# Performance work log

Hardware: AMD Instinct MI355X
Metric: run time of the kernel (lower is better)

The kernel has to match this reference:

```python
import jax, jax.numpy as jnp
import numpy as np

E, TOPK = 32, 2            # hardcoded in LossMOEDecoder
D, HID, BOT, OUT = 768, 2048, 256, 768
B, S = 2, 128


def setup_inputs() -> dict:
    key = jax.random.key(0)
    ks = jax.random.split(key, 7)
    p = lambda k, shape: jax.random.normal(k, shape, dtype=jnp.float32) * 0.02
    return {
        "x": jax.random.normal(ks[0], (B, S, D), dtype=jnp.float32),
        "gate_w": p(ks[1], (E, D)),                 # MoEGate.weight
        "W1": p(ks[2], (E, D, HID)),  "b1": jnp.zeros((E, HID), jnp.float32),
        "W2": p(ks[3], (E, HID, HID)), "b2": jnp.zeros((E, HID), jnp.float32),
        "W3": p(ks[4], (E, HID, BOT)), "b3": jnp.zeros((E, BOT), jnp.float32),
        "Wl": p(ks[5], (E, BOT, OUT)), "bl": jnp.zeros((E, OUT), jnp.float32),
    }


def reference(x, gate_w, W1, b1, W2, b2, W3, b3, Wl, bl):
    Bz, Sl, d = x.shape
    xt = x.reshape(-1, d)                                    # [N, d] tokens
    # --- gate: softmax then top-k (values permutation-invariant vs torch sorted=False)
    scores = jax.nn.softmax(xt @ gate_w.T, axis=-1)          # [N, E]
    topk_w, topk_idx = jax.lax.top_k(scores, TOPK)           # [N, k]
    topk_w = topk_w / (topk_w.sum(-1, keepdims=True) + 1e-20)  # norm_topk_prob
    # --- experts: batched over the (small, fixed) expert axis; exact GELU as nn.GELU
    gelu = lambda v: jax.nn.gelu(v, approximate=False)
    h = gelu(jnp.einsum('nd,edh->enh', xt, W1) + b1[:, None, :])   # [E, N, HID]
    h = gelu(jnp.einsum('enh,ehg->eng', h, W2) + b2[:, None, :])   # [E, N, HID]
    z = jnp.einsum('eng,egb->enb', h, W3) + b3[:, None, :]         # [E, N, BOT]
    out_all = jnp.einsum('enb,ebo->eno', z, Wl) + bl[:, None, :]   # [E, N, OUT]
    # --- combine: gather each token's top-k expert outputs, weighted sum
    sel = jnp.take_along_axis(out_all.transpose(1, 0, 2),          # [N, E, OUT]
                              topk_idx[:, :, None], axis=1)        # [N, k, OUT]
    y = (sel * topk_w[:, :, None]).sum(axis=1)                     # [N, OUT]
    return y.reshape(Bz, Sl, OUT)
```

## Files before the change

### kernel.cpp

```cpp
#include <hip/hip_runtime.h>
#include <math.h>

#define NEXP 32
#define NTOK 256
#define DIMD 768
#define DHID 2048
#define DBOT 256
#define DOUT 768
#define NSLOT 512

__global__ __launch_bounds__(64) void gate_kernel(
    const float* __restrict__ x, const float* __restrict__ gw,
    int* __restrict__ topk_idx, float* __restrict__ topk_w) {
  const int n = blockIdx.x;
  const int l = threadIdx.x;
  const float* xr = x + n * DIMD;
  float xs[12];
#pragma unroll
  for (int j = 0; j < 12; j++) xs[j] = xr[l + 64 * j];
  float logit[NEXP];
#pragma unroll
  for (int e = 0; e < NEXP; e++) {
    const float* g = gw + e * DIMD;
    float p = 0.f;
#pragma unroll
    for (int j = 0; j < 12; j++) p = fmaf(xs[j], g[l + 64 * j], p);
#pragma unroll
    for (int m = 1; m < 64; m <<= 1) p += __shfl_xor(p, m);
    logit[e] = p;
  }
  int i0 = 0; float m0 = logit[0];
#pragma unroll
  for (int e = 1; e < NEXP; e++) { if (logit[e] > m0) { m0 = logit[e]; i0 = e; } }
  int i1 = -1; float m1 = -3.4e38f;
#pragma unroll
  for (int e = 0; e < NEXP; e++) { if (e != i0 && logit[e] > m1) { m1 = logit[e]; i1 = e; } }
  const float e1 = expf(m1 - m0);
  const float w0 = 1.f / (1.f + e1);
  const float w1 = e1 * w0;
  if (l == 0) {
    topk_idx[2 * n] = i0; topk_idx[2 * n + 1] = i1;
    topk_w[2 * n] = w0;  topk_w[2 * n + 1] = w1;
  }
}

__global__ __launch_bounds__(256) void build_lists(
    const int* __restrict__ topk_idx,
    int* __restrict__ counts, int* __restrict__ offsets,
    int* __restrict__ tok_list, int* __restrict__ tok2slot,
    int* __restrict__ slot_expert) {
  __shared__ int cnt[NEXP], base[NEXP], fill[NEXP];
  const int t = threadIdx.x;
  if (t < NEXP) { cnt[t] = 0; fill[t] = 0; }
  __syncthreads();
  const int e0 = topk_idx[2 * t], e1 = topk_idx[2 * t + 1];
  atomicAdd(&cnt[e0], 1);
  atomicAdd(&cnt[e1], 1);
  __syncthreads();
  if (t == 0) { int s = 0; for (int i = 0; i < NEXP; i++) { base[i] = s; s += cnt[i]; } }
  __syncthreads();
  const int p0 = atomicAdd(&fill[e0], 1);
  tok_list[base[e0] + p0] = t; tok2slot[2 * t] = base[e0] + p0;
  slot_expert[base[e0] + p0] = e0;
  const int p1 = atomicAdd(&fill[e1], 1);
  tok_list[base[e1] + p1] = t; tok2slot[2 * t + 1] = base[e1] + p1;
  slot_expert[base[e1] + p1] = e1;
  if (t < NEXP) { counts[t] = cnt[t]; offsets[t] = base[t]; }
}

__device__ __forceinline__ float gelu_f(float v) {
  return 0.5f * v * (1.f + erff(v * 0.70710678118654752f));
}

__global__ __launch_bounds__(64) void zsum_kernel(
    const float* __restrict__ zpart, const float* __restrict__ b3,
    const int* __restrict__ slot_expert, float* __restrict__ zsum) {
  const int slot = blockIdx.x;
  const int c = threadIdx.x * 4;
  const int e = slot_expert[slot];
  float4 q = *(const float4*)(b3 + (size_t)e * DBOT + c);
#pragma unroll
  for (int k = 0; k < 8; k++) {
    const float4 p = *(const float4*)(zpart + ((size_t)k * NSLOT + slot) * DBOT + c);
    q.x += p.x; q.y += p.y; q.z += p.z; q.w += p.w;
  }
  *(float4*)(zsum + (size_t)slot * DBOT + c) = q;
}

#define FMA4(A, XS, WV) \
  A.x = fmaf(XS, WV.x, A.x); A.y = fmaf(XS, WV.y, A.y); \
  A.z = fmaf(XS, WV.z, A.z); A.w = fmaf(XS, WV.w, A.w)

template <int MODE>
__global__ __launch_bounds__(512, 2) void ff_kernel(
    const float* __restrict__ Ain, const float* __restrict__ W,
    const float* __restrict__ Bias, float* __restrict__ Out,
    const int* __restrict__ offsets, const int* __restrict__ counts,
    const int* __restrict__ tok_list) {
  constexpr int NCT   = (MODE <= 1) ? 2048 : (MODE == 2) ? 256 : 768;
  constexpr int KFULL = (MODE == 0) ? 768 : (MODE == 3) ? 256 : 2048;
  constexpr int INS   = (MODE == 0) ? DIMD : (MODE == 3) ? DBOT : DHID;
  constexpr int NSEC  = (MODE == 0) ? 12 : (MODE == 1) ? 32 : 4;
  __shared__ float Wlds[2 * 64 * 256];
  __shared__ float act_t[2 * 64 * 32];
  const int tid  = threadIdx.x;
  const int lane = tid & 63;
  const int wave = tid >> 6;
  const int tg   = wave;
  const int e    = blockIdx.y;
  const int kb   = (MODE == 2) ? blockIdx.x : 0;
  const int ct   = (MODE == 2) ? 0 : blockIdx.x;
  const int kbase = kb * 256;
  const int cnt = counts[e];
  const int off = offsets[e];
  const int col = ct * 256 + lane * 4;
  const float* Wsrc = W + ((size_t)e * KFULL) * NCT + (size_t)ct * 256;
  const int tok = tid & 31;
  const int kk  = tid >> 5;

  for (int tc0 = 0; tc0 < cnt; tc0 += 32) {
    const int tcn = min(32, cnt - tc0);
    const int slot = off + tc0 + tok;
    const float* Arow = nullptr;
    if (tok < tcn) {
      const int row = (MODE == 0) ? tok_list[slot] : slot;
      Arow = Ain + (size_t)row * INS + kbase;
    }

    float4 acc[4];
#pragma unroll
    for (int t = 0; t < 4; t++) acc[t] = {0.f, 0.f, 0.f, 0.f};
    float4 av = {0.f, 0.f, 0.f, 0.f};

    auto a_issue = [&](int s) {
      if (Arow) av = *(const float4*)(Arow + s * 64 + kk * 4);
      else      av = {0.f, 0.f, 0.f, 0.f};
    };
    auto w_issue = [&](int b, int s) {
      float* wl = Wlds + b * 16384;
      const float* src = Wsrc + (size_t)(kbase + s * 64) * NCT;
#pragma unroll
      for (int c = 0; c < 8; c++) {
        const int r = c * 8 + wave;
        __builtin_amdgcn_global_load_lds(
            (const __attribute__((address_space(1))) void*)(src + (size_t)r * NCT + lane * 4),
            (__attribute__((address_space(3))) void*)(wl + r * 256),
            16, 0, 0);
      }
    };
    auto a_write = [&](int b) {
      float* at = act_t + b * 2048;
      at[(kk * 4 + 0) * 32 + tok] = av.x;
      at[(kk * 4 + 1) * 32 + tok] = av.y;
      at[(kk * 4 + 2) * 32 + tok] = av.z;
      at[(kk * 4 + 3) * 32 + tok] = av.w;
    };

    a_issue(0);
    w_issue(0, 0);
    a_write(0);
    __syncthreads();

    for (int s = 0; s < NSEC; s++) {
      const int b = s & 1;
      if (s + 1 < NSEC) {
        a_issue(s + 1);
        w_issue(b ^ 1, s + 1);
      }
      {
        const float* wl = Wlds + b * 16384 + lane * 4;
        const float* at = act_t + b * 2048 + tg * 4;
#pragma unroll 8
        for (int r = 0; r < 64; r++) {
          const float4 wv = *(const float4*)(wl + r * 256);
          const float4 xv = *(const float4*)(at + r * 32);
          FMA4(acc[0], xv.x, wv);
          FMA4(acc[1], xv.y, wv);
          FMA4(acc[2], xv.z, wv);
          FMA4(acc[3], xv.w, wv);
        }
      }
      if (s + 1 < NSEC) a_write(b ^ 1);
      __syncthreads();
    }

    float4 bv = {0.f, 0.f, 0.f, 0.f};
    if (MODE <= 1) bv = *(const float4*)(Bias + (size_t)e * NCT + col);
#pragma unroll
    for (int tt = 0; tt < 4; tt++) {
      if (tg * 4 + tt < tcn) {
        const int os = off + tc0 + tg * 4 + tt;
        float4 o = acc[tt];
        if (MODE <= 1) {
          o.x = gelu_f(o.x + bv.x); o.y = gelu_f(o.y + bv.y);
          o.z = gelu_f(o.z + bv.z); o.w = gelu_f(o.w + bv.w);
          *(float4*)(Out + (size_t)os * NCT + col) = o;
        } else if (MODE == 2) {
          *(float4*)(Out + ((size_t)kb * NSLOT + os) * DBOT + col) = o;
        } else {
          *(float4*)(Out + (size_t)os * DOUT + col) = o;
        }
      }
    }
    __syncthreads();
  }
}

__global__ __launch_bounds__(192) void combine_kernel(
    const float* __restrict__ OutS, const float* __restrict__ bl,
    const int* __restrict__ topk_idx, const float* __restrict__ topk_w,
    const int* __restrict__ tok2slot, float* __restrict__ y) {
  const int n = blockIdx.x;
  const int c = threadIdx.x * 4;
  const int s0 = tok2slot[2 * n], s1 = tok2slot[2 * n + 1];
  const int e0 = topk_idx[2 * n], e1 = topk_idx[2 * n + 1];
  const float w0 = topk_w[2 * n], w1 = topk_w[2 * n + 1];
  const float4 a  = *(const float4*)(OutS + (size_t)s0 * DOUT + c);
  const float4 b  = *(const float4*)(OutS + (size_t)s1 * DOUT + c);
  const float4 ba = *(const float4*)(bl + (size_t)e0 * DOUT + c);
  const float4 bb = *(const float4*)(bl + (size_t)e1 * DOUT + c);
  float4 o;
  o.x = w0 * (a.x + ba.x) + w1 * (b.x + bb.x);
  o.y = w0 * (a.y + ba.y) + w1 * (b.y + bb.y);
  o.z = w0 * (a.z + ba.z) + w1 * (b.z + bb.z);
  o.w = w0 * (a.w + ba.w) + w1 * (b.w + bb.w);
  *(float4*)(y + (size_t)n * DOUT + c) = o;
}

extern "C" void kernel_launch(void* const* d_in, const int* in_sizes, int n_in,
                              void* d_out, int out_size, void* d_ws, size_t ws_size,
                              hipStream_t stream) {
  const float* x  = (const float*)d_in[0];
  const float* gw = (const float*)d_in[1];
  const float* W1 = (const float*)d_in[2];
  const float* b1 = (const float*)d_in[3];
  const float* W2 = (const float*)d_in[4];
  const float* b2 = (const float*)d_in[5];
  const float* W3 = (const float*)d_in[6];
  const float* b3 = (const float*)d_in[7];
  const float* Wl = (const float*)d_in[8];
  const float* bl = (const float*)d_in[9];
  float* y  = (float*)d_out;
  float* ws = (float*)d_ws;

  float* topk_w   = ws;
  int*   topk_idx = (int*)(ws + 512);
  int*   counts   = (int*)(ws + 1024);
  int*   offsets  = (int*)(ws + 1056);
  int*   tok_list = (int*)(ws + 1088);
  int*   tok2slot = (int*)(ws + 1600);
  int*   slot_exp = (int*)(ws + 2112);
  float* B1    = ws + 4096;
  float* B2    = B1 + (size_t)NSLOT * DHID;
  float* zpart = B2 + (size_t)NSLOT * DHID;
  float* zsum  = zpart + (size_t)8 * NSLOT * DBOT;
  float* OutS  = zsum + (size_t)NSLOT * DBOT;

  gate_kernel<<<NTOK, 64, 0, stream>>>(x, gw, topk_idx, topk_w);
  build_lists<<<1, 256, 0, stream>>>(topk_idx, counts, offsets, tok_list, tok2slot, slot_exp);
  ff_kernel<0><<<dim3(8, 32), 512, 0, stream>>>(x,  W1, b1, B1, offsets, counts, tok_list);
  ff_kernel<1><<<dim3(8, 32), 512, 0, stream>>>(B1, W2, b2, B2, offsets, counts, tok_list);
  ff_kernel<2><<<dim3(8, 32), 512, 0, stream>>>(B2, W3, nullptr, zpart, offsets, counts, tok_list);
  zsum_kernel<<<NSLOT, 64, 0, stream>>>(zpart, b3, slot_exp, zsum);
  ff_kernel<3><<<dim3(3, 32), 512, 0, stream>>>(zsum, Wl, nullptr, OutS, offsets, counts, tok_list);
  combine_kernel<<<NTOK, 192, 0, stream>>>(OutS, bl, topk_idx, topk_w, tok2slot, y);
}
```

Measured before the change: 401.4 us.

## Fuse split-K partial reduction into final FF stage and halve block size

Removes the separate zsum kernel: the last feed-forward stage now sums the 8 split-K partials plus the b3 bias while loading its activation tiles, so slot_expert is no longer needed. The FF kernel also drops from 512 to 256 threads per block, with each wave computing 8 tokens instead of 4, which doubles the register tile and the work per thread. This saves one kernel launch and one intermediate round trip through global memory, but each block now has half as many waves to hide latency, and the fused stage re-reads the partials for every column tile (3x).

Measured after the change: 460.6 us. 14.8% more time.

```diff
diff --git a/kernel.cpp b/kernel.cpp
--- a/kernel.cpp
+++ b/kernel.cpp
@@ -47,8 +47,7 @@
 __global__ __launch_bounds__(256) void build_lists(
     const int* __restrict__ topk_idx,
     int* __restrict__ counts, int* __restrict__ offsets,
-    int* __restrict__ tok_list, int* __restrict__ tok2slot,
-    int* __restrict__ slot_expert) {
+    int* __restrict__ tok_list, int* __restrict__ tok2slot) {
   __shared__ int cnt[NEXP], base[NEXP], fill[NEXP];
   const int t = threadIdx.x;
   if (t < NEXP) { cnt[t] = 0; fill[t] = 0; }
@@ -61,52 +60,36 @@
   __syncthreads();
   const int p0 = atomicAdd(&fill[e0], 1);
   tok_list[base[e0] + p0] = t; tok2slot[2 * t] = base[e0] + p0;
-  slot_expert[base[e0] + p0] = e0;
   const int p1 = atomicAdd(&fill[e1], 1);
   tok_list[base[e1] + p1] = t; tok2slot[2 * t + 1] = base[e1] + p1;
-  slot_expert[base[e1] + p1] = e1;
   if (t < NEXP) { counts[t] = cnt[t]; offsets[t] = base[t]; }
 }
 
 __device__ __forceinline__ float gelu_f(float v) {
   return 0.5f * v * (1.f + erff(v * 0.70710678118654752f));
-}
-
-__global__ __launch_bounds__(64) void zsum_kernel(
-    const float* __restrict__ zpart, const float* __restrict__ b3,
-    const int* __restrict__ slot_expert, float* __restrict__ zsum) {
-  const int slot = blockIdx.x;
-  const int c = threadIdx.x * 4;
-  const int e = slot_expert[slot];
-  float4 q = *(const float4*)(b3 + (size_t)e * DBOT + c);
-#pragma unroll
-  for (int k = 0; k < 8; k++) {
-    const float4 p = *(const float4*)(zpart + ((size_t)k * NSLOT + slot) * DBOT + c);
-    q.x += p.x; q.y += p.y; q.z += p.z; q.w += p.w;
-  }
-  *(float4*)(zsum + (size_t)slot * DBOT + c) = q;
 }
 
 #define FMA4(A, XS, WV) \
   A.x = fmaf(XS, WV.x, A.x); A.y = fmaf(XS, WV.y, A.y); \
   A.z = fmaf(XS, WV.z, A.z); A.w = fmaf(XS, WV.w, A.w)
+#define ADD4(Q, P) Q.x += P.x; Q.y += P.y; Q.z += P.z; Q.w += P.w
 
 template <int MODE>
-__global__ __launch_bounds__(512, 2) void ff_kernel(
+__global__ __launch_bounds__(256) void ff_kernel(
     const float* __restrict__ Ain, const float* __restrict__ W,
     const float* __restrict__ Bias, float* __restrict__ Out,
+    const float* __restrict__ zpart,
     const int* __restrict__ offsets, const int* __restrict__ counts,
     const int* __restrict__ tok_list) {
   constexpr int NCT   = (MODE <= 1) ? 2048 : (MODE == 2) ? 256 : 768;
   constexpr int KFULL = (MODE == 0) ? 768 : (MODE == 3) ? 256 : 2048;
-  constexpr int INS   = (MODE == 0) ? DIMD : (MODE == 3) ? DBOT : DHID;
+  constexpr int INS   = (MODE == 0) ? DIMD : DHID;
   constexpr int NSEC  = (MODE == 0) ? 12 : (MODE == 1) ? 32 : 4;
   __shared__ float Wlds[2 * 64 * 256];
   __shared__ float act_t[2 * 64 * 32];
   const int tid  = threadIdx.x;
   const int lane = tid & 63;
   const int wave = tid >> 6;
-  const int tg   = wave;
   const int e    = blockIdx.y;
   const int kb   = (MODE == 2) ? blockIdx.x : 0;
   const int ct   = (MODE == 2) ? 0 : blockIdx.x;
@@ -114,34 +97,56 @@
   const int cnt = counts[e];
   const int off = offsets[e];
   const int col = ct * 256 + lane * 4;
-  const float* Wsrc = W + ((size_t)e * KFULL) * NCT + (size_t)ct * 256;
-  const int tok = tid & 31;
-  const int kk  = tid >> 5;
+  const float* Wsrc = W + (size_t)e * KFULL * NCT + (size_t)ct * 256;
+  const int tok  = tid & 31;
+  const int kseg = tid >> 5;
 
   for (int tc0 = 0; tc0 < cnt; tc0 += 32) {
     const int tcn = min(32, cnt - tc0);
     const int slot = off + tc0 + tok;
     const float* Arow = nullptr;
-    if (tok < tcn) {
+    if (tok < tcn && MODE != 3) {
       const int row = (MODE == 0) ? tok_list[slot] : slot;
       Arow = Ain + (size_t)row * INS + kbase;
     }
 
-    float4 acc[4];
-#pragma unroll
-    for (int t = 0; t < 4; t++) acc[t] = {0.f, 0.f, 0.f, 0.f};
-    float4 av = {0.f, 0.f, 0.f, 0.f};
+    float4 acc[8];
+#pragma unroll
+    for (int t = 0; t < 8; t++) acc[t] = {0.f, 0.f, 0.f, 0.f};
+    float4 av0 = {0.f, 0.f, 0.f, 0.f}, av1 = {0.f, 0.f, 0.f, 0.f};
 
     auto a_issue = [&](int s) {
-      if (Arow) av = *(const float4*)(Arow + s * 64 + kk * 4);
-      else      av = {0.f, 0.f, 0.f, 0.f};
+      const int base = s * 64 + kseg * 8;
+      if (MODE == 3) {
+        if (tok < tcn) {
+          float4 q0 = *(const float4*)(Bias + (size_t)e * DBOT + base);
+          float4 q1 = *(const float4*)(Bias + (size_t)e * DBOT + base + 4);
+#pragma unroll
+          for (int k = 0; k < 8; k++) {
+            const float* zp = zpart + ((size_t)k * NSLOT + slot) * DBOT + base;
+            const float4 p0 = *(const float4*)(zp);
+            const float4 p1 = *(const float4*)(zp + 4);
+            ADD4(q0, p0); ADD4(q1, p1);
+          }
+          av0 = q0; av1 = q1;
+        } else {
+          av0 = {0.f, 0.f, 0.f, 0.f}; av1 = {0.f, 0.f, 0.f, 0.f};
+        }
+      } else {
+        if (Arow) {
+          av0 = *(const float4*)(Arow + base);
+          av1 = *(const float4*)(Arow + base + 4);
+        } else {
+          av0 = {0.f, 0.f, 0.f, 0.f}; av1 = {0.f, 0.f, 0.f, 0.f};
+        }
+      }
     };
     auto w_issue = [&](int b, int s) {
       float* wl = Wlds + b * 16384;
       const float* src = Wsrc + (size_t)(kbase + s * 64) * NCT;
 #pragma unroll
-      for (int c = 0; c < 8; c++) {
-        const int r = c * 8 + wave;
+      for (int c = 0; c < 16; c++) {
+        const int r = c * 4 + wave;
         __builtin_amdgcn_global_load_lds(
             (const __attribute__((address_space(1))) void*)(src + (size_t)r * NCT + lane * 4),
             (__attribute__((address_space(3))) void*)(wl + r * 256),
@@ -150,10 +155,14 @@
     };
     auto a_write = [&](int b) {
       float* at = act_t + b * 2048;
-      at[(kk * 4 + 0) * 32 + tok] = av.x;
-      at[(kk * 4 + 1) * 32 + tok] = av.y;
-      at[(kk * 4 + 2) * 32 + tok] = av.z;
-      at[(kk * 4 + 3) * 32 + tok] = av.w;
+      at[(kseg * 8 + 0) * 32 + tok] = av0.x;
+      at[(kseg * 8 + 1) * 32 + tok] = av0.y;
+      at[(kseg * 8 + 2) * 32 + tok] = av0.z;
+      at[(kseg * 8 + 3) * 32 + tok] = av0.w;
+      at[(kseg * 8 + 4) * 32 + tok] = av1.x;
+      at[(kseg * 8 + 5) * 32 + tok] = av1.y;
+      at[(kseg * 8 + 6) * 32 + tok] = av1.z;
+      at[(kseg * 8 + 7) * 32 + tok] = av1.w;
     };
 
     a_issue(0);
@@ -169,15 +178,20 @@
       }
       {
         const float* wl = Wlds + b * 16384 + lane * 4;
-        const float* at = act_t + b * 2048 + tg * 4;
+        const float* at = act_t + b * 2048 + wave * 8;
 #pragma unroll 8
         for (int r = 0; r < 64; r++) {
           const float4 wv = *(const float4*)(wl + r * 256);
-          const float4 xv = *(const float4*)(at + r * 32);
-          FMA4(acc[0], xv.x, wv);
-          FMA4(acc[1], xv.y, wv);
-          FMA4(acc[2], xv.z, wv);
-          FMA4(acc[3], xv.w, wv);
+          const float4 x0 = *(const float4*)(at + r * 32);
+          const float4 x1 = *(const float4*)(at + r * 32 + 4);
+          FMA4(acc[0], x0.x, wv);
+          FMA4(acc[1], x0.y, wv);
+          FMA4(acc[2], x0.z, wv);
+          FMA4(acc[3], x0.w, wv);
+          FMA4(acc[4], x1.x, wv);
+          FMA4(acc[5], x1.y, wv);
+          FMA4(acc[6], x1.z, wv);
+          FMA4(acc[7], x1.w, wv);
         }
       }
       if (s + 1 < NSEC) a_write(b ^ 1);
@@ -187,16 +201,16 @@
     float4 bv = {0.f, 0.f, 0.f, 0.f};
     if (MODE <= 1) bv = *(const float4*)(Bias + (size_t)e * NCT + col);
 #pragma unroll
-    for (int tt = 0; tt < 4; tt++) {
-      if (tg * 4 + tt < tcn) {
-        const int os = off + tc0 + tg * 4 + tt;
+    for (int tt = 0; tt < 8; tt++) {
+      if (wave * 8 + tt < tcn) {
+        const int os = off + tc0 + wave * 8 + tt;
         float4 o = acc[tt];
         if (MODE <= 1) {
           o.x = gelu_f(o.x + bv.x); o.y = gelu_f(o.y + bv.y);
           o.z = gelu_f(o.z + bv.z); o.w = gelu_f(o.w + bv.w);
           *(float4*)(Out + (size_t)os * NCT + col) = o;
         } else if (MODE == 2) {
-          *(float4*)(Out + ((size_t)kb * NSLOT + os) * DBOT + col) = o;
+          *(float4*)(Out + ((size_t)kb * NSLOT + os) * DBOT + lane * 4) = o;
         } else {
           *(float4*)(Out + (size_t)os * DOUT + col) = o;
         }
@@ -249,19 +263,20 @@
   int*   offsets  = (int*)(ws + 1056);
   int*   tok_list = (int*)(ws + 1088);
   int*   tok2slot = (int*)(ws + 1600);
-  int*   slot_exp = (int*)(ws + 2112);
   float* B1    = ws + 4096;
   float* B2    = B1 + (size_t)NSLOT * DHID;
   float* zpart = B2 + (size_t)NSLOT * DHID;
-  float* zsum  = zpart + (size_t)8 * NSLOT * DBOT;
-  float* OutS  = zsum + (size_t)NSLOT * DBOT;
+  float* OutS  = zpart + (size_t)8 * NSLOT * DBOT;
 
   gate_kernel<<<NTOK, 64, 0, stream>>>(x, gw, topk_idx, topk_w);
-  build_lists<<<1, 256, 0, stream>>>(topk_idx, counts, offsets, tok_list, tok2slot, slot_exp);
-  ff_kernel<0><<<dim3(8, 32), 512, 0, stream>>>(x,  W1, b1, B1, offsets, counts, tok_list);
-  ff_kernel<1><<<dim3(8, 32), 512, 0, stream>>>(B1, W2, b2, B2, offsets, counts, tok_list);
-  ff_kernel<2><<<dim3(8, 32), 512, 0, stream>>>(B2, W3, nullptr, zpart, offsets, counts, tok_list);
-  zsum_kernel<<<NSLOT, 64, 0, stream>>>(zpart, b3, slot_exp, zsum);
-  ff_kernel<3><<<dim3(3, 32), 512, 0, stream>>>(zsum, Wl, nullptr, OutS, offsets, counts, tok_list);
+  build_lists<<<1, 256, 0, stream>>>(topk_idx, counts, offsets, tok_list, tok2slot);
+  ff_kernel<0><<<dim3(8, 32), 256, 0, stream>>>(x,  W1, b1, B1, nullptr,
+                                                offsets, counts, tok_list);
+  ff_kernel<1><<<dim3(8, 32), 256, 0, stream>>>(B1, W2, b2, B2, nullptr,
+                                                offsets, counts, tok_list);
+  ff_kernel<2><<<dim3(8, 32), 256, 0, stream>>>(B2, W3, nullptr, zpart, nullptr,
+                                                offsets, counts, tok_list);
+  ff_kernel<3><<<dim3(3, 32), 256, 0, stream>>>(nullptr, Wl, b3, OutS, zpart,
+                                                offsets, counts, tok_list);
   combine_kernel<<<NTOK, 192, 0, stream>>>(OutS, bl, topk_idx, topk_w, tok2slot, y);
 }
```

## Split-K all expert FF layers in two and reduce partials in separate kernels

Applied to the files above, without the earlier changes.

Every expert matmul is now split along K into two halves, which doubles the grid to 16x32 (6x32 for the last layer) so more CUs are busy. The partial sums go to workspace and are reduced by new h_combine kernels that add bias and apply GELU, and the final combine sums two partials. LDS tiles shrink from 64 to 32 rows per stage to raise occupancy. The cost is extra launches and extra global traffic for the partial buffers.

Measured after the change: 424.5 us. 5.8% more time.

```diff
diff --git a/kernel.cpp b/kernel.cpp
--- a/kernel.cpp
+++ b/kernel.cpp
@@ -72,6 +72,136 @@
   return 0.5f * v * (1.f + erff(v * 0.70710678118654752f));
 }
 
+#define FMA4(A, XS, WV) \
+  A.x = fmaf(XS, WV.x, A.x); A.y = fmaf(XS, WV.y, A.y); \
+  A.z = fmaf(XS, WV.z, A.z); A.w = fmaf(XS, WV.w, A.w)
+#define ADD4(Q, P) Q.x += P.x; Q.y += P.y; Q.z += P.z; Q.w += P.w
+
+template <int MODE>
+__global__ __launch_bounds__(512, 2) void ff_kernel(
+    const float* __restrict__ Ain, const float* __restrict__ W,
+    float* __restrict__ Out,
+    const int* __restrict__ offsets, const int* __restrict__ counts,
+    const int* __restrict__ tok_list) {
+  constexpr int NCT   = (MODE <= 1) ? 2048 : (MODE == 2) ? 256 : 768;
+  constexpr int KBLK  = (MODE == 0) ? 384 : (MODE == 1) ? 1024 : 128;
+  constexpr int NSEC  = KBLK / 32;
+  constexpr int KFULL = (MODE == 0) ? 768 : (MODE == 3) ? 256 : 2048;
+  constexpr int INS   = (MODE == 0) ? DIMD : (MODE == 3) ? DBOT : DHID;
+  constexpr int CT    = (MODE <= 1) ? 8 : (MODE == 2) ? 1 : 3;
+  __shared__ float Wlds[2 * 32 * 256];
+  __shared__ float act_t[2 * 32 * 32];
+  const int tid  = threadIdx.x;
+  const int lane = tid & 63;
+  const int wave = tid >> 6;
+  const int e    = blockIdx.y;
+  const int ct   = blockIdx.x % CT;
+  const int kb   = blockIdx.x / CT;
+  const int kbase = kb * KBLK;
+  const int cnt = counts[e];
+  const int off = offsets[e];
+  const int col = ct * 256 + lane * 4;
+  const float* Wsrc = W + (size_t)e * KFULL * NCT + (size_t)ct * 256;
+  float* Outp = Out + (size_t)kb * NSLOT * NCT;
+  const int tok  = tid & 31;
+  const int kseg = tid >> 5;
+
+  for (int tc0 = 0; tc0 < cnt; tc0 += 32) {
+    const int tcn = min(32, cnt - tc0);
+    const int slot = off + tc0 + tok;
+    const float* Arow = nullptr;
+    if (tok < tcn) {
+      const int row = (MODE == 0) ? tok_list[slot] : slot;
+      Arow = Ain + (size_t)row * INS + kbase;
+    }
+
+    float4 acc[4];
+#pragma unroll
+    for (int t = 0; t < 4; t++) acc[t] = {0.f, 0.f, 0.f, 0.f};
+
+    auto a_load = [&](int s) -> float2 {
+      if (Arow) return *(const float2*)(Arow + s * 32 + kseg * 2);
+      return {0.f, 0.f};
+    };
+    auto w_issue = [&](int b, int s) {
+      float* wl = Wlds + b * 8192;
+      const float* src = Wsrc + (size_t)(kbase + s * 32) * NCT;
+#pragma unroll
+      for (int c = 0; c < 4; c++) {
+        const int r = c * 8 + wave;
+        __builtin_amdgcn_global_load_lds(
+            (const __attribute__((address_space(1))) void*)(src + (size_t)r * NCT + lane * 4),
+            (__attribute__((address_space(3))) void*)(wl + r * 256),
+            16, 0, 0);
+      }
+    };
+    auto a_write = [&](int b, float2 v) {
+      float* at = act_t + b * 1024;
+      at[(kseg * 2 + 0) * 32 + tok] = v.x;
+      at[(kseg * 2 + 1) * 32 + tok] = v.y;
+    };
+
+    {
+      float2 v0 = a_load(0);
+      w_issue(0, 0);
+      a_write(0, v0);
+    }
+    __syncthreads();
+
+    for (int s = 0; s < NSEC; s++) {
+      const int b = s & 1;
+      float2 vn;
+      if (s + 1 < NSEC) {
+        vn = a_load(s + 1);
+        w_issue(b ^ 1, s + 1);
+      }
+      {
+        const float* wl = Wlds + b * 8192 + lane * 4;
+        const float* at = act_t + b * 1024 + wave * 4;
+#pragma unroll 8
+        for (int r = 0; r < 32; r++) {
+          const float4 wv = *(const float4*)(wl + r * 256);
+          const float4 xv = *(const float4*)(at + r * 32);
+          FMA4(acc[0], xv.x, wv);
+          FMA4(acc[1], xv.y, wv);
+          FMA4(acc[2], xv.z, wv);
+          FMA4(acc[3], xv.w, wv);
+        }
+      }
+      if (s + 1 < NSEC) a_write(b ^ 1, vn);
+      __syncthreads();
+    }
+
+#pragma unroll
+    for (int tt = 0; tt < 4; tt++) {
+      if (wave * 4 + tt < tcn) {
+        const int os = off + tc0 + wave * 4 + tt;
+        *(float4*)(Outp + (size_t)os * NCT + col) = acc[tt];
+      }
+    }
+    __syncthreads();
+  }
+}
+
+__global__ __launch_bounds__(256) void h_combine(
+    const float* __restrict__ P0, const float* __restrict__ P1,
+    const float* __restrict__ bias, const int* __restrict__ slot_expert,
+    float* __restrict__ Bout) {
+  const int slot = blockIdx.x;
+  const int e = slot_expert[slot];
+  const int c0 = threadIdx.x * 8;
+#pragma unroll
+  for (int j = 0; j < 8; j += 4) {
+    float4 a = *(const float4*)(P0 + (size_t)slot * DHID + c0 + j);
+    const float4 b = *(const float4*)(P1 + (size_t)slot * DHID + c0 + j);
+    const float4 bb = *(const float4*)(bias + (size_t)e * DHID + c0 + j);
+    float4 o;
+    o.x = gelu_f(a.x + b.x + bb.x); o.y = gelu_f(a.y + b.y + bb.y);
+    o.z = gelu_f(a.z + b.z + bb.z); o.w = gelu_f(a.w + b.w + bb.w);
+    *(float4*)(Bout + (size_t)slot * DHID + c0 + j) = o;
+  }
+}
+
 __global__ __launch_bounds__(64) void zsum_kernel(
     const float* __restrict__ zpart, const float* __restrict__ b3,
     const int* __restrict__ slot_expert, float* __restrict__ zsum) {
@@ -80,134 +210,16 @@
   const int e = slot_expert[slot];
   float4 q = *(const float4*)(b3 + (size_t)e * DBOT + c);
 #pragma unroll
-  for (int k = 0; k < 8; k++) {
+  for (int k = 0; k < 16; k++) {
     const float4 p = *(const float4*)(zpart + ((size_t)k * NSLOT + slot) * DBOT + c);
-    q.x += p.x; q.y += p.y; q.z += p.z; q.w += p.w;
+    ADD4(q, p);
   }
   *(float4*)(zsum + (size_t)slot * DBOT + c) = q;
 }
 
-#define FMA4(A, XS, WV) \
-  A.x = fmaf(XS, WV.x, A.x); A.y = fmaf(XS, WV.y, A.y); \
-  A.z = fmaf(XS, WV.z, A.z); A.w = fmaf(XS, WV.w, A.w)
-
-template <int MODE>
-__global__ __launch_bounds__(512, 2) void ff_kernel(
-    const float* __restrict__ Ain, const float* __restrict__ W,
-    const float* __restrict__ Bias, float* __restrict__ Out,
-    const int* __restrict__ offsets, const int* __restrict__ counts,
-    const int* __restrict__ tok_list) {
-  constexpr int NCT   = (MODE <= 1) ? 2048 : (MODE == 2) ? 256 : 768;
-  constexpr int KFULL = (MODE == 0) ? 768 : (MODE == 3) ? 256 : 2048;
-  constexpr int INS   = (MODE == 0) ? DIMD : (MODE == 3) ? DBOT : DHID;
-  constexpr int NSEC  = (MODE == 0) ? 12 : (MODE == 1) ? 32 : 4;
-  __shared__ float Wlds[2 * 64 * 256];
-  __shared__ float act_t[2 * 64 * 32];
-  const int tid  = threadIdx.x;
-  const int lane = tid & 63;
-  const int wave = tid >> 6;
-  const int tg   = wave;
-  const int e    = blockIdx.y;
-  const int kb   = (MODE == 2) ? blockIdx.x : 0;
-  const int ct   = (MODE == 2) ? 0 : blockIdx.x;
-  const int kbase = kb * 256;
-  const int cnt = counts[e];
-  const int off = offsets[e];
-  const int col = ct * 256 + lane * 4;
-  const float* Wsrc = W + ((size_t)e * KFULL) * NCT + (size_t)ct * 256;
-  const int tok = tid & 31;
-  const int kk  = tid >> 5;
-
-  for (int tc0 = 0; tc0 < cnt; tc0 += 32) {
-    const int tcn = min(32, cnt - tc0);
-    const int slot = off + tc0 + tok;
-    const float* Arow = nullptr;
-    if (tok < tcn) {
-      const int row = (MODE == 0) ? tok_list[slot] : slot;
-      Arow = Ain + (size_t)row * INS + kbase;
-    }
-
-    float4 acc[4];
-#pragma unroll
-    for (int t = 0; t < 4; t++) acc[t] = {0.f, 0.f, 0.f, 0.f};
-    float4 av = {0.f, 0.f, 0.f, 0.f};
-
-    auto a_issue = [&](int s) {
-      if (Arow) av = *(const float4*)(Arow + s * 64 + kk * 4);
-      else      av = {0.f, 0.f, 0.f, 0.f};
-    };
-    auto w_issue = [&](int b, int s) {
-      float* wl = Wlds + b * 16384;
-      const float* src = Wsrc + (size_t)(kbase + s * 64) * NCT;
-#pragma unroll
-      for (int c = 0; c < 8; c++) {
-        const int r = c * 8 + wave;
-        __builtin_amdgcn_global_load_lds(
-            (const __attribute__((address_space(1))) void*)(src + (size_t)r * NCT + lane * 4),
-            (__attribute__((address_space(3))) void*)(wl + r * 256),
-            16, 0, 0);
-      }
-    };
-    auto a_write = [&](int b) {
-      float* at = act_t + b * 2048;
-      at[(kk * 4 + 0) * 32 + tok] = av.x;
-      at[(kk * 4 + 1) * 32 + tok] = av.y;
-      at[(kk * 4 + 2) * 32 + tok] = av.z;
-      at[(kk * 4 + 3) * 32 + tok] = av.w;
-    };
-
-    a_issue(0);
-    w_issue(0, 0);
-    a_write(0);
-    __syncthreads();
-
-    for (int s = 0; s < NSEC; s++) {
-      const int b = s & 1;
-      if (s + 1 < NSEC) {
-        a_issue(s + 1);
-        w_issue(b ^ 1, s + 1);
-      }
-      {
-        const float* wl = Wlds + b * 16384 + lane * 4;
-        const float* at = act_t + b * 2048 + tg * 4;
-#pragma unroll 8
-        for (int r = 0; r < 64; r++) {
-          const float4 wv = *(const float4*)(wl + r * 256);
-          const float4 xv = *(const float4*)(at + r * 32);
-          FMA4(acc[0], xv.x, wv);
-          FMA4(acc[1], xv.y, wv);
-          FMA4(acc[2], xv.z, wv);
-          FMA4(acc[3], xv.w, wv);
-        }
-      }
-      if (s + 1 < NSEC) a_write(b ^ 1);
-      __syncthreads();
-    }
-
-    float4 bv = {0.f, 0.f, 0.f, 0.f};
-    if (MODE <= 1) bv = *(const float4*)(Bias + (size_t)e * NCT + col);
-#pragma unroll
-    for (int tt = 0; tt < 4; tt++) {
-      if (tg * 4 + tt < tcn) {
-        const int os = off + tc0 + tg * 4 + tt;
-        float4 o = acc[tt];
-        if (MODE <= 1) {
-          o.x = gelu_f(o.x + bv.x); o.y = gelu_f(o.y + bv.y);
-          o.z = gelu_f(o.z + bv.z); o.w = gelu_f(o.w + bv.w);
-          *(float4*)(Out + (size_t)os * NCT + col) = o;
-        } else if (MODE == 2) {
-          *(float4*)(Out + ((size_t)kb * NSLOT + os) * DBOT + col) = o;
-        } else {
-          *(float4*)(Out + (size_t)os * DOUT + col) = o;
-        }
-      }
-    }
-    __syncthreads();
-  }
-}
-
 __global__ __launch_bounds__(192) void combine_kernel(
-    const float* __restrict__ OutS, const float* __restrict__ bl,
+    const float* __restrict__ OP0, const float* __restrict__ OP1,
+    const float* __restrict__ bl,
     const int* __restrict__ topk_idx, const float* __restrict__ topk_w,
     const int* __restrict__ tok2slot, float* __restrict__ y) {
   const int n = blockIdx.x;
@@ -215,15 +227,17 @@
   const int s0 = tok2slot[2 * n], s1 = tok2slot[2 * n + 1];
   const int e0 = topk_idx[2 * n], e1 = topk_idx[2 * n + 1];
   const float w0 = topk_w[2 * n], w1 = topk_w[2 * n + 1];
-  const float4 a  = *(const float4*)(OutS + (size_t)s0 * DOUT + c);
-  const float4 b  = *(const float4*)(OutS + (size_t)s1 * DOUT + c);
+  float4 a = *(const float4*)(OP0 + (size_t)s0 * DOUT + c);
+  const float4 a1 = *(const float4*)(OP1 + (size_t)s0 * DOUT + c);
   const float4 ba = *(const float4*)(bl + (size_t)e0 * DOUT + c);
+  float4 b = *(const float4*)(OP0 + (size_t)s1 * DOUT + c);
+  const float4 b1 = *(const float4*)(OP1 + (size_t)s1 * DOUT + c);
   const float4 bb = *(const float4*)(bl + (size_t)e1 * DOUT + c);
   float4 o;
-  o.x = w0 * (a.x + ba.x) + w1 * (b.x + bb.x);
-  o.y = w0 * (a.y + ba.y) + w1 * (b.y + bb.y);
-  o.z = w0 * (a.z + ba.z) + w1 * (b.z + bb.z);
-  o.w = w0 * (a.w + ba.w) + w1 * (b.w + bb.w);
+  o.x = w0 * (a.x + a1.x + ba.x) + w1 * (b.x + b1.x + bb.x);
+  o.y = w0 * (a.y + a1.y + ba.y) + w1 * (b.y + b1.y + bb.y);
+  o.z = w0 * (a.z + a1.z + ba.z) + w1 * (b.z + b1.z + bb.z);
+  o.w = w0 * (a.w + a1.w + ba.w) + w1 * (b.w + b1.w + bb.w);
   *(float4*)(y + (size_t)n * DOUT + c) = o;
 }
 
@@ -250,18 +264,24 @@
   int*   tok_list = (int*)(ws + 1088);
   int*   tok2slot = (int*)(ws + 1600);
   int*   slot_exp = (int*)(ws + 2112);
-  float* B1    = ws + 4096;
-  float* B2    = B1 + (size_t)NSLOT * DHID;
-  float* zpart = B2 + (size_t)NSLOT * DHID;
-  float* zsum  = zpart + (size_t)8 * NSLOT * DBOT;
-  float* OutS  = zsum + (size_t)NSLOT * DBOT;
+  const size_t M = (size_t)NSLOT * DHID;
+  float* B1p   = ws + 4096;
+  float* B1    = B1p + 2 * M;
+  float* B2p   = B1 + M;
+  float* B2    = B2p + 2 * M;
+  float* zpart = B2 + M;
+  float* zsum  = zpart + (size_t)16 * NSLOT * DBOT;
+  float* OutSp = zsum + (size_t)NSLOT * DBOT;
 
   gate_kernel<<<NTOK, 64, 0, stream>>>(x, gw, topk_idx, topk_w);
   build_lists<<<1, 256, 0, stream>>>(topk_idx, counts, offsets, tok_list, tok2slot, slot_exp);
-  ff_kernel<0><<<dim3(8, 32), 512, 0, stream>>>(x,  W1, b1, B1, offsets, counts, tok_list);
-  ff_kernel<1><<<dim3(8, 32), 512, 0, stream>>>(B1, W2, b2, B2, offsets, counts, tok_list);
-  ff_kernel<2><<<dim3(8, 32), 512, 0, stream>>>(B2, W3, nullptr, zpart, offsets, counts, tok_list);
+  ff_kernel<0><<<dim3(16, 32), 512, 0, stream>>>(x, W1, B1p, offsets, counts, tok_list);
+  h_combine<<<NSLOT, 256, 0, stream>>>(B1p, B1p + M, b1, slot_exp, B1);
+  ff_kernel<1><<<dim3(16, 32), 512, 0, stream>>>(B1, W2, B2p, offsets, counts, tok_list);
+  h_combine<<<NSLOT, 256, 0, stream>>>(B2p, B2p + M, b2, slot_exp, B2);
+  ff_kernel<2><<<dim3(16, 32), 512, 0, stream>>>(B2, W3, zpart, offsets, counts, tok_list);
   zsum_kernel<<<NSLOT, 64, 0, stream>>>(zpart, b3, slot_exp, zsum);
-  ff_kernel<3><<<dim3(3, 32), 512, 0, stream>>>(zsum, Wl, nullptr, OutS, offsets, counts, tok_list);
-  combine_kernel<<<NTOK, 192, 0, stream>>>(OutS, bl, topk_idx, topk_w, tok2slot, y);
-}
+  ff_kernel<3><<<dim3(6, 32), 512, 0, stream>>>(zsum, Wl, OutSp, offsets, counts, tok_list);
+  combine_kernel<<<NTOK, 192, 0, stream>>>(OutSp, OutSp + (size_t)NSLOT * DOUT, bl,
+                                           topk_idx, topk_w, tok2slot, y);
+}
```
